# Optimization experiments

Hardware: AMD Instinct MI355X
Metric: run time of the kernel (lower is better)

The kernel has to match this reference:

```python
import jax, jax.numpy as jnp
import numpy as np

B, N, C, PH, PW = 16, 256, 1, 16, 16
G, HID = 8, 256
TEMP = 0.5
EPS = 1e-5


def setup_inputs() -> dict:
    key = jax.random.key(0)
    ks = jax.random.split(key, 16)
    f32 = jnp.float32
    def kaiming(k, shape):  # fan_out mode for convs, OIHW
        fan_out = shape[0] * shape[2] * shape[3]
        return jax.random.normal(k, shape, f32) * np.float32(np.sqrt(2.0 / fan_out))
    def lin(k, shape):  # nn.init.normal_(w, 0, 0.01)
        return jax.random.normal(k, shape, f32) * np.float32(0.01)
    return {
        "x": jax.random.normal(ks[0], (B, N, C, PH, PW), f32),
        "conv1_w": kaiming(ks[1], (32, 1, 3, 3)),  "conv1_b": jnp.zeros((32,), f32),
        "bn1_g": jnp.ones((32,), f32),  "bn1_b": jnp.zeros((32,), f32),
        "conv2_w": kaiming(ks[2], (64, 32, 3, 3)), "conv2_b": jnp.zeros((64,), f32),
        "bn2_g": jnp.ones((64,), f32),  "bn2_b": jnp.zeros((64,), f32),
        "conv3_w": kaiming(ks[3], (128, 64, 3, 3)), "conv3_b": jnp.zeros((128,), f32),
        "bn3_g": jnp.ones((128,), f32), "bn3_b": jnp.zeros((128,), f32),
        "fc_w": lin(ks[4], (HID, 128)),       "fc_b": jnp.zeros((HID,), f32),
        "g1_w": lin(ks[5], (2 * HID, HID)),   "g1_b": jnp.zeros((2 * HID,), f32),
        "ln1_g": jnp.ones((2 * HID,), f32),   "ln1_b": jnp.zeros((2 * HID,), f32),
        "g2_w": lin(ks[6], (2 * HID, 2 * HID)), "g2_b": jnp.zeros((2 * HID,), f32),
        "ln2_g": jnp.ones((2 * HID,), f32),   "ln2_b": jnp.zeros((2 * HID,), f32),
        "g3_w": lin(ks[7], (G, 2 * HID)),     "g3_b": jnp.zeros((G,), f32),
    }


def _conv(h, w, b):
    out = jax.lax.conv_general_dilated(h, w, (1, 1), 'SAME',
        dimension_numbers=('NCHW', 'OIHW', 'NCHW'))
    return out + b[None, :, None, None]


def _bn_train(h, g, b):  # batch stats over (N, H, W), biased variance
    m = h.mean(axis=(0, 2, 3), keepdims=True)
    v = h.var(axis=(0, 2, 3), keepdims=True)
    return (h - m) * jax.lax.rsqrt(v + EPS) * g[None, :, None, None] + b[None, :, None, None]


def _ln(h, g, b):
    m = h.mean(axis=-1, keepdims=True)
    v = h.var(axis=-1, keepdims=True)
    return (h - m) * jax.lax.rsqrt(v + EPS) * g + b


def reference(x, conv1_w, conv1_b, bn1_g, bn1_b, conv2_w, conv2_b, bn2_g, bn2_b,
              conv3_w, conv3_b, bn3_g, bn3_b, fc_w, fc_b,
              g1_w, g1_b, ln1_g, ln1_b, g2_w, g2_b, ln2_g, ln2_b, g3_w, g3_b):
    Bx, Nx, Cx, ph, pw = x.shape
    Gx = g3_w.shape[0]
    K = Nx // Gx  # num_patches_per_group

    # ---- patch encoder (conv + BN(train) + ReLU x3, GAP, Linear) ----
    h = x.reshape(Bx * Nx, Cx, ph, pw)
    h = jax.nn.relu(_bn_train(_conv(h, conv1_w, conv1_b), bn1_g, bn1_b))
    h = jax.nn.relu(_bn_train(_conv(h, conv2_w, conv2_b), bn2_g, bn2_b))
    h = jax.nn.relu(_bn_train(_conv(h, conv3_w, conv3_b), bn3_g, bn3_b))
    feat = h.mean(axis=(2, 3))                     # [B*N, 128] (AdaptiveAvgPool2d(1))
    feat = feat @ fc_w.T + fc_b                    # [B*N, HID]
    feat = feat.reshape(Bx, Nx, -1)

    # ---- grouping network ----
    h = jax.nn.relu(_ln(feat @ g1_w.T + g1_b, ln1_g, ln1_b))
    h = jax.nn.relu(_ln(h @ g2_w.T + g2_b, ln2_g, ln2_b))
    logits = (h @ g3_w.T + g3_b) / TEMP            # [B, N, G]
    assignment = jax.nn.softmax(logits, axis=2)    # [B, N, G]

    # ---- per-group top-K weighted patch gather (training path) ----
    w = jnp.transpose(assignment, (0, 2, 1))       # [B, G, N]
    vals, idx = jax.lax.top_k(w, K)                # [B, G, K] (descending, matches sort)
    idx_e = idx[:, :, :, None, None, None]         # [B, G, K, 1, 1, 1]
    gathered = jnp.take_along_axis(x[:, None], idx_e, axis=2)  # [B, G, K, C, ph, pw]
    output = gathered * vals[:, :, :, None, None, None]
    return output, assignment
```

## Files before the change

### kernel.cpp

```cpp
#include <hip/hip_runtime.h>


typedef float f32x16 __attribute__((ext_vector_type(16)));

#define WS_W1   0
#define WS_B1   288
#define WS_W2   320
#define WS_B2   18752
#define WS_W3   18816
#define WS_B3   92544
#define WS_FCW  92672
#define WS_FCB  125440
#define WS_G1W  125696
#define WS_G1B  256768
#define WS_L1G  257280
#define WS_L1B  257792
#define WS_G2W  258304
#define WS_G2B  520448
#define WS_L2G  520960
#define WS_L2B  521472
#define WS_G3W  521984
#define WS_G3B  526080
#define D_ACC1  263044
#define D_ACC2  (D_ACC1 + 4096)
#define D_ACC3  (D_ACC2 + 8192)
#define D_FEAT  (D_ACC3 + 16384)
#define D_AFF1  (D_FEAT + 524288)
#define D_AFF2  (D_AFF1 + 64)
#define D_AFF3  (D_AFF2 + 128)
#define D_ZN    553408
#define Z2_OFF_B 6532096ull


__global__ __launch_bounds__(256) void k_zero(double* __restrict__ dst){
  int i = blockIdx.x*256 + threadIdx.x;
  if(i < D_ZN) dst[i] = 0.0;
}

struct WP { const float* p[18]; };

__global__ __launch_bounds__(256) void k_cvt(WP wp, float* __restrict__ dst){
  const int segn[18] = {288,32,18432,64,73728,128,32768,256,131072,512,512,512,262144,512,512,512,4096,8};
  const int sego[18] = {WS_W1,WS_B1,WS_W2,WS_B2,WS_W3,WS_B3,WS_FCW,WS_FCB,WS_G1W,WS_G1B,
                        WS_L1G,WS_L1B,WS_G2W,WS_G2B,WS_L2G,WS_L2B,WS_G3W,WS_G3B};
  int s = blockIdx.y;
  int i = blockIdx.x*256 + threadIdx.x;
  if(i < segn[s]){
    if(s == 4){
      int oc = i / 576;
      int rem = i - oc*576;
      int ic = rem / 9;
      int j  = rem - ic*9;
      dst[WS_W3 + ic*1152 + j*128 + oc] = wp.p[4][i];
    } else {
      dst[sego[s]+i] = wp.p[s][i];
    }
  }
}

__global__ __launch_bounds__(64) void k_fin(const double* __restrict__ acc, int C,
                                            const float* __restrict__ gam, const float* __restrict__ bet,
                                            double* __restrict__ aff){
  int c = blockIdx.x, t = threadIdx.x;
  double s = acc[t*2*C + c*2];
  double q = acc[t*2*C + c*2 + 1];
  #pragma unroll
  for(int off=32;off;off>>=1){ s += __shfl_down(s,off); q += __shfl_down(q,off); }
  if(t==0){
    double m = s*(1.0/1048576.0);
    double v = q*(1.0/1048576.0) - m*m;
    double sc = (double)gam[c] / sqrt(v + 1e-5);
    aff[2*c]   = sc;
    aff[2*c+1] = (double)bet[c] - m*sc;
  }
}

__global__ __launch_bounds__(256) void k_p1(const float* __restrict__ x, const float* __restrict__ wf,
                                            double* __restrict__ acc1){
  __shared__ float xp[324];
  __shared__ double red[4][32][2];
  int p = blockIdx.x, t = threadIdx.x;
  for(int i=t;i<324;i+=256) xp[i]=0.f;
  __syncthreads();
  int py=t>>4, px=t&15;
  xp[(py+1)*18 + px + 1] = x[(size_t)p*256+t];
  __syncthreads();
  float nb[9];
  #pragma unroll
  for(int j=0;j<9;j++) nb[j] = xp[(py+j/3)*18 + px + (j%3)];
  int wave=t>>6, lane=t&63;
  for(int c=0;c<32;c++){
    float a = wf[WS_B1+c];
    #pragma unroll
    for(int j=0;j<9;j++) a = fmaf(nb[j], wf[WS_W1+c*9+j], a);
    double av=(double)a;
    double s=av, q=av*av;
    #pragma unroll
    for(int off=32;off;off>>=1){ s+=__shfl_down(s,off); q+=__shfl_down(q,off); }
    if(lane==0){ red[wave][c][0]=s; red[wave][c][1]=q; }
  }
  __syncthreads();
  if(t<64){
    int c=t>>1, st=t&1;
    double v = red[0][c][st]+red[1][c][st]+red[2][c][st]+red[3][c][st];
    atomicAdd(&acc1[(p&63)*64 + c*2 + st], v);
  }
}

__global__ __launch_bounds__(256) void k_p2(const float* __restrict__ x, const float* __restrict__ wf,
                                            const double* __restrict__ aff1, double* __restrict__ acc2,
                                            float* __restrict__ z2, int nS){
  __shared__ float xp[324];
  __shared__ float h1f[32*324];
  int p=blockIdx.x, t=threadIdx.x;
  for(int i=t;i<324;i+=256) xp[i]=0.f;
  for(int i=t;i<32*324;i+=256) h1f[i]=0.f;
  __syncthreads();
  int py=t>>4, px=t&15;
  xp[(py+1)*18 + px + 1] = x[(size_t)p*256+t];
  __syncthreads();
  {
    float nb[9];
    #pragma unroll
    for(int j=0;j<9;j++) nb[j] = xp[(py+j/3)*18 + px + (j%3)];
    for(int c=0;c<32;c++){
      float a = wf[WS_B1+c];
      #pragma unroll
      for(int j=0;j<9;j++) a = fmaf(nb[j], wf[WS_W1+c*9+j], a);
      h1f[c*324 + (py+1)*18 + (px+1)] = fmaxf(fmaf((float)aff1[2*c], a, (float)aff1[2*c+1]), 0.f);
    }
  }
  __syncthreads();
  int col=t&15, og=t>>4;
  bool wr = (p < nS);
  double sT[4]={0,0,0,0}, qT[4]={0,0,0,0};
  #pragma unroll 1
  for(int half=0; half<2; ++half){
    float acc[4][8];
    #pragma unroll
    for(int o=0;o<4;o++){
      float bv = wf[WS_B2 + og*4 + o];
      #pragma unroll
      for(int r=0;r<8;r++) acc[o][r]=bv;
    }
    #pragma unroll 1
    for(int ic=0; ic<32; ++ic){
      const float* wrow = wf + WS_W2 + (og*4*32 + ic)*9;
      #pragma unroll
      for(int j=0;j<9;j++){
        float w4[4];
        #pragma unroll
        for(int o=0;o<4;o++) w4[o] = wrow[o*288 + j];
        int dy=j/3, dx=j%3;
        #pragma unroll
        for(int r=0;r<8;r++){
          float m = h1f[ic*324 + (half*8 + r + dy)*18 + col + dx];
          #pragma unroll
          for(int o=0;o<4;o++) acc[o][r] = fmaf(m, w4[o], acc[o][r]);
        }
      }
    }
    #pragma unroll
    for(int o=0;o<4;o++){
      #pragma unroll
      for(int r=0;r<8;r++){ double v=(double)acc[o][r]; sT[o]+=v; qT[o]+=v*v; }
      if(wr){
        int c = og*4+o;
        #pragma unroll
        for(int r=0;r<8;r++) z2[((size_t)p*64+c)*256 + (half*8+r)*16 + col] = acc[o][r];
      }
    }
  }
  #pragma unroll
  for(int o=0;o<4;o++){
    double s=sT[o], q=qT[o];
    #pragma unroll
    for(int off=8;off;off>>=1){ s+=__shfl_down(s,off,16); q+=__shfl_down(q,off,16); }
    if(col==0){
      int c = og*4+o;
      atomicAdd(&acc2[(p&63)*128 + c*2 + 0], s);
      atomicAdd(&acc2[(p&63)*128 + c*2 + 1], q);
    }
  }
}

__global__ __launch_bounds__(512) void k_cs(const float* __restrict__ wf, const double* __restrict__ aff2,
                                            double* __restrict__ acc3, const float* __restrict__ z2){
  __shared__ float h2S[32*200];
  int bid=blockIdx.x, t=threadIdx.x;
  int p = bid>>1, r0 = (bid&1)*8;
  for(int i=t;i<6400;i+=512) h2S[i]=0.f;
  int col=t&15, q=(t>>4)&3;
  int wv = __builtin_amdgcn_readfirstlane(t>>6);
  float acc[16][2];
  #pragma unroll
  for(int o=0;o<16;o++){
    float bv = wf[WS_B3 + wv*16 + o];
    acc[o][0]=bv; acc[o][1]=bv;
  }
  const f32x16* wW = reinterpret_cast<const f32x16*>(wf + WS_W3 + wv*16);
  #pragma unroll 1
  for(int half=0; half<2; ++half){
    __syncthreads();
    for(int i=t;i<5120;i+=512){
      int ch2 = i/160, rem = i - ch2*160;
      int row = rem>>4, c2 = rem&15;
      int gr = r0 - 1 + row;
      if(gr>=0 && gr<16){
        int ch = half*32 + ch2;
        float zv = z2[((size_t)p*64+ch)*256 + gr*16 + c2];
        h2S[ch2*200 + row*20 + c2+1] = fmaxf(fmaf((float)aff2[2*ch], zv, (float)aff2[2*ch+1]), 0.f);
      }
    }
    __syncthreads();
    #pragma unroll 1
    for(int ic2=0; ic2<32; ++ic2){
      int ic = half*32 + ic2;
      float a[4][3];
      #pragma unroll
      for(int lr=0; lr<4; ++lr){
        #pragma unroll
        for(int dx=0; dx<3; ++dx) a[lr][dx] = h2S[ic2*200 + (2*q+lr)*20 + col + dx];
      }
      #pragma unroll
      for(int j=0;j<9;j++){
        f32x16 w = wW[ic*72 + j*8];
        int dy=j/3, dx=j%3;
        #pragma unroll
        for(int o=0;o<16;o++){
          acc[o][0] = fmaf(a[dy  ][dx], w[o], acc[o][0]);
          acc[o][1] = fmaf(a[dy+1][dx], w[o], acc[o][1]);
        }
      }
    }
  }
  #pragma unroll
  for(int o=0;o<16;o++){
    double s  = (double)acc[o][0] + (double)acc[o][1];
    double q2 = (double)acc[o][0]*(double)acc[o][0] + (double)acc[o][1]*(double)acc[o][1];
    #pragma unroll
    for(int off=32;off;off>>=1){ s += __shfl_down(s,off); q2 += __shfl_down(q2,off); }
    if((t&63)==0){
      int c = wv*16+o;
      atomicAdd(&acc3[(bid&63)*256 + c*2 + 0], s);
      atomicAdd(&acc3[(bid&63)*256 + c*2 + 1], q2);
    }
  }
}

__global__ __launch_bounds__(512) void k_cf(const float* __restrict__ wf, const double* __restrict__ aff2,
                                            const double* __restrict__ aff3, double* __restrict__ feat,
                                            const float* __restrict__ z2){
  __shared__ float h2S[32*200];
  int bid=blockIdx.x, t=threadIdx.x;
  int p = bid>>1, r0 = (bid&1)*8;
  for(int i=t;i<6400;i+=512) h2S[i]=0.f;
  int col=t&15, q=(t>>4)&3;
  int wv = __builtin_amdgcn_readfirstlane(t>>6);
  float acc[16][2];
  #pragma unroll
  for(int o=0;o<16;o++){
    float bv = wf[WS_B3 + wv*16 + o];
    acc[o][0]=bv; acc[o][1]=bv;
  }
  const f32x16* wW = reinterpret_cast<const f32x16*>(wf + WS_W3 + wv*16);
  #pragma unroll 1
  for(int half=0; half<2; ++half){
    __syncthreads();
    for(int i=t;i<5120;i+=512){
      int ch2 = i/160, rem = i - ch2*160;
      int row = rem>>4, c2 = rem&15;
      int gr = r0 - 1 + row;
      if(gr>=0 && gr<16){
        int ch = half*32 + ch2;
        float zv = z2[((size_t)p*64+ch)*256 + gr*16 + c2];
        h2S[ch2*200 + row*20 + c2+1] = fmaxf(fmaf((float)aff2[2*ch], zv, (float)aff2[2*ch+1]), 0.f);
      }
    }
    __syncthreads();
    #pragma unroll 1
    for(int ic2=0; ic2<32; ++ic2){
      int ic = half*32 + ic2;
      float a[4][3];
      #pragma unroll
      for(int lr=0; lr<4; ++lr){
        #pragma unroll
        for(int dx=0; dx<3; ++dx) a[lr][dx] = h2S[ic2*200 + (2*q+lr)*20 + col + dx];
      }
      #pragma unroll
      for(int j=0;j<9;j++){
        f32x16 w = wW[ic*72 + j*8];
        int dy=j/3, dx=j%3;
        #pragma unroll
        for(int o=0;o<16;o++){
          acc[o][0] = fmaf(a[dy  ][dx], w[o], acc[o][0]);
          acc[o][1] = fmaf(a[dy+1][dx], w[o], acc[o][1]);
        }
      }
    }
  }
  #pragma unroll
  for(int o=0;o<16;o++){
    int c = wv*16+o;
    float sc=(float)aff3[2*c], sh=(float)aff3[2*c+1];
    double sv = (double)fmaxf(fmaf(sc, acc[o][0], sh), 0.f)
              + (double)fmaxf(fmaf(sc, acc[o][1], sh), 0.f);
    #pragma unroll
    for(int off=32;off;off>>=1) sv += __shfl_down(sv,off);
    if((t&63)==0) atomicAdd(&feat[(size_t)p*128 + c], sv);
  }
}

__global__ __launch_bounds__(256) void k_stat3(const float* __restrict__ x, const float* __restrict__ wf,
                                               const double* __restrict__ aff1, const double* __restrict__ aff2,
                                               double* __restrict__ acc3, int p0){
  __shared__ float xp[324];
  __shared__ float h1S[32*144];
  __shared__ float h2S[64*108];
  int bid=blockIdx.x, t=threadIdx.x;
  int p = p0 + (bid>>2), r0 = (bid&3)*4;
  for(int i=t;i<64*108;i+=256) h2S[i]=0.f;
  for(int i=t;i<324;i+=256) xp[i]=0.f;
  for(int i=t;i<32*144;i+=256) h1S[i]=0.f;
  __syncthreads();
  { int py=t>>4, px=t&15; xp[(py+1)*18 + px + 1] = x[(size_t)p*256+t]; }
  __syncthreads();
  {
    int rr=t>>5, cw=t&31, col=cw&15, half=cw>>4;
    int p1 = r0-1+rr;
    if(p1>=1 && p1<=16){
      float nb[9];
      #pragma unroll
      for(int j=0;j<9;j++) nb[j] = xp[(p1-1+j/3)*18 + col + (j%3)];
      for(int k=0;k<16;k++){
        int c = half*16+k;
        float a = wf[WS_B1+c];
        #pragma unroll
        for(int j=0;j<9;j++) a = fmaf(nb[j], wf[WS_W1+c*9+j], a);
        h1S[c*144 + rr*18 + col+1] = fmaxf((float)aff1[2*c]*a + (float)aff1[2*c+1], 0.f);
      }
    }
  }
  __syncthreads();
  {
    int col=t&15, g=t>>4;
    float a24[4][6];
    #pragma unroll
    for(int o=0;o<4;o++){
      float bv = wf[WS_B2+g*4+o];
      #pragma unroll
      for(int b2=0;b2<6;b2++) a24[o][b2] = bv;
    }
    #pragma unroll 1
    for(int ic=0;ic<32;ic++){
      const float* wrow = wf + WS_W2 + (g*4*32 + ic)*9;
      #pragma unroll
      for(int j=0;j<9;j++){
        float w4[4];
        #pragma unroll
        for(int o=0;o<4;o++) w4[o] = wrow[o*288 + j];
        int dy=j/3, dx=j%3;
        #pragma unroll
        for(int b2=0;b2<6;b2++){
          float m = h1S[ic*144 + (b2+dy)*18 + col + dx];
          #pragma unroll
          for(int o=0;o<4;o++) a24[o][b2] = fmaf(m, w4[o], a24[o][b2]);
        }
      }
    }
    #pragma unroll
    for(int b2=0;b2<6;b2++){
      int p2 = r0+b2;
      if(p2>=1 && p2<=16){
        #pragma unroll
        for(int o=0;o<4;o++){
          int c=g*4+o;
          h2S[c*108 + b2*18 + col+1] = fmaxf((float)aff2[2*c]*a24[o][b2] + (float)aff2[2*c+1], 0.f);
        }
      }
    }
  }
  __syncthreads();
  {
    int col = t & 15, og = t >> 4;
    float acc[8][4];
    #pragma unroll
    for(int o=0;o<8;o++){
      float bv = wf[WS_B3 + og*8 + o];
      #pragma unroll
      for(int r=0;r<4;r++) acc[o][r] = bv;
    }
    #pragma unroll 1
    for(int ic=0; ic<64; ++ic){
      float a[6][3];
      #pragma unroll
      for(int rr=0; rr<6; ++rr){
        #pragma unroll
        for(int dx=0; dx<3; ++dx) a[rr][dx] = h2S[ic*108 + rr*18 + col + dx];
      }
      const float* wrow = wf + WS_W3 + ic*1152;
      #pragma unroll
      for(int o=0;o<8;o++){
        #pragma unroll
        for(int j=0;j<9;j++){
          float w = wrow[j*128 + og*8 + o];
          #pragma unroll
          for(int r=0;r<4;r++) acc[o][r] = fmaf(a[r + j/3][j%3], w, acc[o][r]);
        }
      }
    }
    #pragma unroll
    for(int o=0;o<8;o++){
      double s=0.0, q=0.0;
      #pragma unroll
      for(int r=0;r<4;r++){ double v=(double)acc[o][r]; s+=v; q+=v*v; }
      #pragma unroll
      for(int off=8; off; off>>=1){ s += __shfl_down(s, off, 16); q += __shfl_down(q, off, 16); }
      if(col==0){
        int c = og*8+o;
        atomicAdd(&acc3[(bid&63)*256 + c*2 + 0], s);
        atomicAdd(&acc3[(bid&63)*256 + c*2 + 1], q);
      }
    }
  }
}

__global__ __launch_bounds__(256) void k_p34(const float* __restrict__ x, const float* __restrict__ wf,
                                             const double* __restrict__ aff1, const double* __restrict__ aff2,
                                             const double* __restrict__ aff3, double* __restrict__ outp,
                                             int p0){
  __shared__ float xp[324];
  __shared__ float h1S[32*144];
  __shared__ float h2S[64*108];
  int bid=blockIdx.x, t=threadIdx.x;
  int p = p0 + (bid>>2), r0 = (bid&3)*4;
  for(int i=t;i<64*108;i+=256) h2S[i]=0.f;
  for(int i=t;i<324;i+=256) xp[i]=0.f;
  for(int i=t;i<32*144;i+=256) h1S[i]=0.f;
  __syncthreads();
  { int py=t>>4, px=t&15; xp[(py+1)*18 + px + 1] = x[(size_t)p*256+t]; }
  __syncthreads();
  {
    int rr=t>>5, cw=t&31, col=cw&15, half=cw>>4;
    int p1 = r0-1+rr;
    if(p1>=1 && p1<=16){
      float nb[9];
      #pragma unroll
      for(int j=0;j<9;j++) nb[j] = xp[(p1-1+j/3)*18 + col + (j%3)];
      for(int k=0;k<16;k++){
        int c = half*16+k;
        float a = wf[WS_B1+c];
        #pragma unroll
        for(int j=0;j<9;j++) a = fmaf(nb[j], wf[WS_W1+c*9+j], a);
        h1S[c*144 + rr*18 + col+1] = fmaxf((float)aff1[2*c]*a + (float)aff1[2*c+1], 0.f);
      }
    }
  }
  __syncthreads();
  {
    int col=t&15, g=t>>4;
    float a24[4][6];
    #pragma unroll
    for(int o=0;o<4;o++){
      float bv = wf[WS_B2+g*4+o];
      #pragma unroll
      for(int b2=0;b2<6;b2++) a24[o][b2] = bv;
    }
    #pragma unroll 1
    for(int ic=0;ic<32;ic++){
      const float* wrow = wf + WS_W2 + (g*4*32 + ic)*9;
      #pragma unroll
      for(int j=0;j<9;j++){
        float w4[4];
        #pragma unroll
        for(int o=0;o<4;o++) w4[o] = wrow[o*288 + j];
        int dy=j/3, dx=j%3;
        #pragma unroll
        for(int b2=0;b2<6;b2++){
          float m = h1S[ic*144 + (b2+dy)*18 + col + dx];
          #pragma unroll
          for(int o=0;o<4;o++) a24[o][b2] = fmaf(m, w4[o], a24[o][b2]);
        }
      }
    }
    #pragma unroll
    for(int b2=0;b2<6;b2++){
      int p2 = r0+b2;
      if(p2>=1 && p2<=16){
        #pragma unroll
        for(int o=0;o<4;o++){
          int c=g*4+o;
          h2S[c*108 + b2*18 + col+1] = fmaxf((float)aff2[2*c]*a24[o][b2] + (float)aff2[2*c+1], 0.f);
        }
      }
    }
  }
  __syncthreads();
  {
    int col = t & 15, og = t >> 4;
    float acc[8][4];
    #pragma unroll
    for(int o=0;o<8;o++){
      float bv = wf[WS_B3 + og*8 + o];
      #pragma unroll
      for(int r=0;r<4;r++) acc[o][r] = bv;
    }
    #pragma unroll 1
    for(int ic=0; ic<64; ++ic){
      float a[6][3];
      #pragma unroll
      for(int rr=0; rr<6; ++rr){
        #pragma unroll
        for(int dx=0; dx<3; ++dx) a[rr][dx] = h2S[ic*108 + rr*18 + col + dx];
      }
      const float* wrow = wf + WS_W3 + ic*1152;
      #pragma unroll
      for(int o=0;o<8;o++){
        #pragma unroll
        for(int j=0;j<9;j++){
          float w = wrow[j*128 + og*8 + o];
          #pragma unroll
          for(int r=0;r<4;r++) acc[o][r] = fmaf(a[r + j/3][j%3], w, acc[o][r]);
        }
      }
    }
    #pragma unroll
    for(int o=0;o<8;o++){
      int c = og*8+o;
      float sc=(float)aff3[2*c], sh=(float)aff3[2*c+1];
      double s = 0.0;
      #pragma unroll
      for(int r=0;r<4;r++) s += (double)fmaxf(fmaf(sc, acc[o][r], sh), 0.f);
      #pragma unroll
      for(int off=8; off; off>>=1) s += __shfl_down(s, off, 16);
      if(col==0) atomicAdd(&outp[(size_t)p*128 + c], s);
    }
  }
}

__device__ __forceinline__ void ln_relu4(double* buf, const float* __restrict__ g, const float* __restrict__ b,
                                         double* lnm, double* lnr, int t){
  int r=t>>6, j=t&63;
  double s=0.0, q=0.0;
  for(int k=j;k<512;k+=64){ double v=buf[r*512+k]; s+=v; q+=v*v; }
  #pragma unroll
  for(int off=32;off;off>>=1){ s+=__shfl_down(s,off); q+=__shfl_down(q,off); }
  if(j==0){
    double m = s*(1.0/512.0);
    double v = q*(1.0/512.0) - m*m;
    lnm[r]=m; lnr[r]=1.0/sqrt(v + 1e-5);
  }
  __syncthreads();
  for(int i=t;i<2048;i+=256){
    int r2=i>>9, k=i&511;
    double v=(buf[i]-lnm[r2])*lnr[r2]*(double)g[k]+(double)b[k];
    buf[i]=fmax(v,0.0);
  }
  __syncthreads();
}

__global__ __launch_bounds__(256) void k_mlp(const float* __restrict__ wf, const double* __restrict__ feat,
                                             float* __restrict__ assign_out){
  int r0 = blockIdx.x*4, t = threadIdx.x;
  __shared__ double f0[4*128];
  __shared__ double f1[4*256];
  __shared__ double f2[4*512];
  __shared__ double f3[4*512];
  __shared__ double lnm[4], lnr[4];
  __shared__ double lg[4][8];

  for(int i=t;i<512;i+=256) f0[i] = feat[(size_t)r0*128 + i] * (1.0/256.0);
  __syncthreads();
  {
    double acc[4];
    double bv = (double)wf[WS_FCB + t];
    #pragma unroll
    for(int r=0;r<4;r++) acc[r]=bv;
    for(int k=0;k<128;k++){
      double wv = (double)wf[WS_FCW + t*128 + k];
      #pragma unroll
      for(int r=0;r<4;r++) acc[r]=fma(wv, f0[r*128+k], acc[r]);
    }
    #pragma unroll
    for(int r=0;r<4;r++) f1[r*256+t]=acc[r];
  }
  __syncthreads();
  for(int half=0;half<2;half++){
    int i=t+(half<<8);
    double acc[4];
    double bv=(double)wf[WS_G1B+i];
    #pragma unroll
    for(int r=0;r<4;r++) acc[r]=bv;
    for(int k=0;k<256;k++){
      double wv=(double)wf[WS_G1W + i*256 + k];
      #pragma unroll
      for(int r=0;r<4;r++) acc[r]=fma(wv, f1[r*256+k], acc[r]);
    }
    #pragma unroll
    for(int r=0;r<4;r++) f2[r*512+i]=acc[r];
  }
  __syncthreads();
  ln_relu4(f2, wf+WS_L1G, wf+WS_L1B, lnm, lnr, t);
  for(int half=0;half<2;half++){
    int i=t+(half<<8);
    double acc[4];
    double bv=(double)wf[WS_G2B+i];
    #pragma unroll
    for(int r=0;r<4;r++) acc[r]=bv;
    for(int k=0;k<512;k++){
      double wv=(double)wf[WS_G2W + i*512 + k];
      #pragma unroll
      for(int r=0;r<4;r++) acc[r]=fma(wv, f2[r*512+k], acc[r]);
    }
    #pragma unroll
    for(int r=0;r<4;r++) f3[r*512+i]=acc[r];
  }
  __syncthreads();
  ln_relu4(f3, wf+WS_L2G, wf+WS_L2B, lnm, lnr, t);
  {
    int r=t>>6, j=t&63;
    double pl[8];
    #pragma unroll
    for(int g=0;g<8;g++){
      double s=0.0;
      for(int k=j;k<512;k+=64) s = fma(f3[r*512+k], (double)wf[WS_G3W + g*512 + k], s);
      pl[g]=s;
    }
    #pragma unroll
    for(int off=32;off;off>>=1){
      #pragma unroll
      for(int g=0;g<8;g++) pl[g] += __shfl_down(pl[g], off);
    }
    if(j==0){
      #pragma unroll
      for(int g=0;g<8;g++) lg[r][g] = (pl[g] + (double)wf[WS_G3B+g]) * 2.0;
    }
  }
  __syncthreads();
  if(t<4){
    double m=-1e300;
    #pragma unroll
    for(int g=0;g<8;g++) m = fmax(m, lg[t][g]);
    double e[8], s=0.0;
    #pragma unroll
    for(int g=0;g<8;g++){ e[g]=exp(lg[t][g]-m); s+=e[g]; }
    double inv = 1.0/s;
    int row = r0 + t;
    #pragma unroll
    for(int g=0;g<8;g++) assign_out[row*8+g] = (float)(e[g]*inv);
  }
}

__global__ __launch_bounds__(256) void k_topk(const float* __restrict__ assign, const float* __restrict__ x,
                                              float* __restrict__ out){
  int b = blockIdx.x >> 3, g = blockIdx.x & 7, t = threadIdx.x;
  __shared__ float v[256];
  __shared__ int   id[256];
  v[t] = assign[(b*256+t)*8 + g];
  id[t] = t;
  __syncthreads();
  for(int k=2;k<=256;k<<=1){
    for(int j=k>>1;j>0;j>>=1){
      int ixj = t ^ j;
      if(ixj > t){
        float va=v[t], vb=v[ixj];
        int ia=id[t], ib=id[ixj];
        bool aBefore = (va > vb) || (va == vb && ia < ib);
        bool up = ((t & k) == 0);
        if(up != aBefore){ v[t]=vb; v[ixj]=va; id[t]=ib; id[ixj]=ia; }
      }
      __syncthreads();
    }
  }
  __shared__ float tv[32];
  __shared__ int   ti[32];
  if(t<32){ tv[t]=v[t]; ti[t]=id[t]; }
  __syncthreads();
  const float* xb = x + (size_t)b*65536;
  float* ob = out + (size_t)(b*8+g)*8192;
  for(int i=t;i<8192;i+=256){
    int k=i>>8, pix=i&255;
    ob[i] = tv[k] * xb[ti[k]*256 + pix];
  }
}

extern "C" void kernel_launch(void* const* d_in, const int* in_sizes, int n_in,
                              void* d_out, int out_size, void* d_ws, size_t ws_size,
                              hipStream_t stream){
  const float* x = (const float*)d_in[0];
  float*  ws  = (float*)d_ws;
  double* dws = (double*)d_ws;
  float* out = (float*)d_out;
  float* assign_out = out + 1048576;
  float* z2 = (float*)((char*)d_ws + Z2_OFF_B);

  int nS = 0;
  if(ws_size > Z2_OFF_B + 65536){
    unsigned long long avail = (unsigned long long)ws_size - Z2_OFF_B;
    unsigned long long n = avail / 65536ull;
    nS = (n > 4096ull) ? 4096 : (int)n;
  }
  int nR = 4096 - nS;

  const float* g1=(const float*)d_in[3];  const float* b1=(const float*)d_in[4];
  const float* g2=(const float*)d_in[7];  const float* b2=(const float*)d_in[8];
  const float* g3=(const float*)d_in[11]; const float* b3=(const float*)d_in[12];

  WP wp;
  const int map[18] = {1,2,5,6,9,10,13,14,15,16,17,18,19,20,21,22,23,24};
  for(int i=0;i<18;i++) wp.p[i] = (const float*)d_in[map[i]];

  k_zero <<<2162, 256, 0, stream>>>(dws + D_ACC1);
  k_cvt  <<<dim3(1024,18), 256, 0, stream>>>(wp, ws);
  k_p1   <<<4096, 256, 0, stream>>>(x, ws, dws+D_ACC1);
  k_fin  <<<32, 64, 0, stream>>>(dws+D_ACC1, 32, g1, b1, dws+D_AFF1);
  k_p2   <<<4096, 256, 0, stream>>>(x, ws, dws+D_AFF1, dws+D_ACC2, z2, nS);
  k_fin  <<<64, 64, 0, stream>>>(dws+D_ACC2, 64, g2, b2, dws+D_AFF2);
  if(nS > 0) k_cs   <<<2*nS, 512, 0, stream>>>(ws, dws+D_AFF2, dws+D_ACC3, z2);
  if(nR > 0) k_stat3<<<4*nR, 256, 0, stream>>>(x, ws, dws+D_AFF1, dws+D_AFF2, dws+D_ACC3, nS);
  k_fin  <<<128, 64, 0, stream>>>(dws+D_ACC3, 128, g3, b3, dws+D_AFF3);
  if(nS > 0) k_cf  <<<2*nS, 512, 0, stream>>>(ws, dws+D_AFF2, dws+D_AFF3, dws+D_FEAT, z2);
  if(nR > 0) k_p34 <<<4*nR, 256, 0, stream>>>(x, ws, dws+D_AFF1, dws+D_AFF2, dws+D_AFF3, dws+D_FEAT, nS);
  k_mlp  <<<1024, 256, 0, stream>>>(ws, dws+D_FEAT, assign_out);
  k_topk <<<128, 256, 0, stream>>>(assign_out, x, out);
}
```

Baseline: 4.040 ms.

## Retile conv2 in k_p2 with wave-uniform transposed weights and register row blocking

Conv2 weights are pre-transposed into an [ic][tap][oc] layout, so each wave loads 16 output-channel weights as one wave-uniform vector. Each thread now computes 16 channels by 4 rows and keeps a 6x3 window of inputs in registers per input channel. This replaces per-thread scattered weight loads and repeated LDS reads. Channel statistics are now reduced with a full-wave shuffle. The cost is higher register pressure from 64 accumulators, which may lower occupancy, plus a larger workspace offset for z2.

```diff
diff --git a/kernel.cpp b/kernel.cpp
--- a/kernel.cpp
+++ b/kernel.cpp
@@ -29,7 +29,8 @@
 #define D_AFF2  (D_AFF1 + 64)
 #define D_AFF3  (D_AFF2 + 128)
 #define D_ZN    553408
-#define Z2_OFF_B 6532096ull
+#define W2T_F   1632912
+#define Z2_OFF_B 6605824ull
 
 
 __global__ __launch_bounds__(256) void k_zero(double* __restrict__ dst){
@@ -40,11 +41,21 @@
 struct WP { const float* p[18]; };
 
 __global__ __launch_bounds__(256) void k_cvt(WP wp, float* __restrict__ dst){
+  int s = blockIdx.y;
+  int i = blockIdx.x*256 + threadIdx.x;
+  if(s == 18){
+    if(i < 18432){
+      int oc = i / 288;
+      int rem = i - oc*288;
+      int ic = rem / 9;
+      int j  = rem - ic*9;
+      dst[W2T_F + ic*576 + j*64 + oc] = wp.p[2][i];
+    }
+    return;
+  }
   const int segn[18] = {288,32,18432,64,73728,128,32768,256,131072,512,512,512,262144,512,512,512,4096,8};
   const int sego[18] = {WS_W1,WS_B1,WS_W2,WS_B2,WS_W3,WS_B3,WS_FCW,WS_FCB,WS_G1W,WS_G1B,
                         WS_L1G,WS_L1B,WS_G2W,WS_G2B,WS_L2G,WS_L2B,WS_G3W,WS_G3B};
-  int s = blockIdx.y;
-  int i = blockIdx.x*256 + threadIdx.x;
   if(i < segn[s]){
     if(s == 4){
       int oc = i / 576;
@@ -131,53 +142,49 @@
     }
   }
   __syncthreads();
-  int col=t&15, og=t>>4;
+  int col=t&15, rq=(t>>4)&3;
+  int wv = __builtin_amdgcn_readfirstlane(t>>6);
+  float acc[16][4];
+  #pragma unroll
+  for(int o=0;o<16;o++){
+    float bv = wf[WS_B2 + wv*16 + o];
+    #pragma unroll
+    for(int r=0;r<4;r++) acc[o][r]=bv;
+  }
+  const f32x16* W2v = reinterpret_cast<const f32x16*>(wf + W2T_F + wv*16);
+  #pragma unroll 1
+  for(int ic=0; ic<32; ++ic){
+    float a[6][3];
+    #pragma unroll
+    for(int lr=0; lr<6; ++lr){
+      #pragma unroll
+      for(int dx=0; dx<3; ++dx) a[lr][dx] = h1f[ic*324 + (4*rq+lr)*18 + col + dx];
+    }
+    #pragma unroll
+    for(int j=0;j<9;j++){
+      f32x16 w = W2v[(ic*9 + j)*4];
+      int dy=j/3, dx=j%3;
+      #pragma unroll
+      for(int o=0;o<16;o++){
+        #pragma unroll
+        for(int r=0;r<4;r++) acc[o][r] = fmaf(a[r+dy][dx], w[o], acc[o][r]);
+      }
+    }
+  }
   bool wr = (p < nS);
-  double sT[4]={0,0,0,0}, qT[4]={0,0,0,0};
-  #pragma unroll 1
-  for(int half=0; half<2; ++half){
-    float acc[4][8];
-    #pragma unroll
-    for(int o=0;o<4;o++){
-      float bv = wf[WS_B2 + og*4 + o];
-      #pragma unroll
-      for(int r=0;r<8;r++) acc[o][r]=bv;
-    }
-    #pragma unroll 1
-    for(int ic=0; ic<32; ++ic){
-      const float* wrow = wf + WS_W2 + (og*4*32 + ic)*9;
-      #pragma unroll
-      for(int j=0;j<9;j++){
-        float w4[4];
-        #pragma unroll
-        for(int o=0;o<4;o++) w4[o] = wrow[o*288 + j];
-        int dy=j/3, dx=j%3;
-        #pragma unroll
-        for(int r=0;r<8;r++){
-          float m = h1f[ic*324 + (half*8 + r + dy)*18 + col + dx];
-          #pragma unroll
-          for(int o=0;o<4;o++) acc[o][r] = fmaf(m, w4[o], acc[o][r]);
-        }
-      }
-    }
-    #pragma unroll
-    for(int o=0;o<4;o++){
-      #pragma unroll
-      for(int r=0;r<8;r++){ double v=(double)acc[o][r]; sT[o]+=v; qT[o]+=v*v; }
-      if(wr){
-        int c = og*4+o;
-        #pragma unroll
-        for(int r=0;r<8;r++) z2[((size_t)p*64+c)*256 + (half*8+r)*16 + col] = acc[o][r];
-      }
-    }
-  }
-  #pragma unroll
-  for(int o=0;o<4;o++){
-    double s=sT[o], q=qT[o];
-    #pragma unroll
-    for(int off=8;off;off>>=1){ s+=__shfl_down(s,off,16); q+=__shfl_down(q,off,16); }
-    if(col==0){
-      int c = og*4+o;
+  #pragma unroll
+  for(int o=0;o<16;o++){
+    int c = wv*16+o;
+    if(wr){
+      #pragma unroll
+      for(int r=0;r<4;r++) z2[((size_t)p*64+c)*256 + (4*rq+r)*16 + col] = acc[o][r];
+    }
+    double s=0.0, q=0.0;
+    #pragma unroll
+    for(int r=0;r<4;r++){ double v=(double)acc[o][r]; s+=v; q+=v*v; }
+    #pragma unroll
+    for(int off=32;off;off>>=1){ s += __shfl_down(s,off); q += __shfl_down(q,off); }
+    if((t&63)==0){
       atomicAdd(&acc2[(p&63)*128 + c*2 + 0], s);
       atomicAdd(&acc2[(p&63)*128 + c*2 + 1], q);
     }
@@ -711,7 +718,7 @@
   for(int i=0;i<18;i++) wp.p[i] = (const float*)d_in[map[i]];
 
   k_zero <<<2162, 256, 0, stream>>>(dws + D_ACC1);
-  k_cvt  <<<dim3(1024,18), 256, 0, stream>>>(wp, ws);
+  k_cvt  <<<dim3(1024,19), 256, 0, stream>>>(wp, ws);
   k_p1   <<<4096, 256, 0, stream>>>(x, ws, dws+D_ACC1);
   k_fin  <<<32, 64, 0, stream>>>(dws+D_ACC1, 32, g1, b1, dws+D_AFF1);
   k_p2   <<<4096, 256, 0, stream>>>(x, ws, dws+D_AFF1, dws+D_ACC2, z2, nS);
```

Measured after the change: 3.975 ms (median of 2 runs). About the same (-1.6%).
